# Kernel tuning notes

Measured on AMD Instinct MI355X. Metric: run time of the kernel, lower is better.

The kernel has to match this reference:

```python
import jax, jax.numpy as jnp
import numpy as np

N, E, F_IN, HID, H, NCLS, L = 100000, 1600000, 128, 128, 4, 40, 2
C = HID // H  # per-head channels = 32
LN_EPS = 1e-5
SOFTMAX_EPS = 1e-16  # PyG softmax denominator epsilon


def setup_inputs() -> dict:
    key = jax.random.key(0)
    ks = jax.random.split(key, 8)
    s = 1.0 / np.sqrt(F_IN).astype(np.float32)
    return {
        "x": jax.random.normal(ks[0], (N, F_IN), jnp.float32),
        "edge_index": jax.random.randint(ks[1], (2, E), 0, N, jnp.int32),
        "Wq": jax.random.normal(ks[2], (L, F_IN, HID), jnp.float32) * s,
        "bq": jnp.zeros((L, HID), jnp.float32),
        "Wk": jax.random.normal(ks[3], (L, F_IN, HID), jnp.float32) * s,
        "bk": jnp.zeros((L, HID), jnp.float32),
        "Wv": jax.random.normal(ks[4], (L, F_IN, HID), jnp.float32) * s,
        "bv": jnp.zeros((L, HID), jnp.float32),
        "Ws": jax.random.normal(ks[5], (L, F_IN, HID), jnp.float32) * s,
        "bs": jnp.zeros((L, HID), jnp.float32),
        "gamma": jnp.ones((L, HID), jnp.float32),
        "beta": jnp.zeros((L, HID), jnp.float32),
        "Wout": jax.random.normal(ks[6], (HID, NCLS), jnp.float32) * (1.0 / np.sqrt(HID).astype(np.float32)),
        "bout": jnp.zeros((NCLS,), jnp.float32),
    }


def _transformer_conv(x, src, dst, Wq, bq, Wk, bk, Wv, bv, Ws, bs):
    # PyG TransformerConv, concat=False, root_weight=True, beta=False
    n = x.shape[0]
    q = (x @ Wq + bq).reshape(n, H, C)
    k = (x @ Wk + bk).reshape(n, H, C)
    v = (x @ Wv + bv).reshape(n, H, C)
    # per-edge attention logits: [E, H]
    alpha = jnp.einsum('ehc,ehc->eh', q[dst], k[src]) / np.sqrt(C).astype(np.float32)
    # segment softmax over incoming edges of each destination node
    amax = jax.ops.segment_max(alpha, dst, num_segments=n)        # [N, H]
    ex = jnp.exp(alpha - amax[dst])                               # [E, H]
    denom = jax.ops.segment_sum(ex, dst, num_segments=n)         # [N, H]
    w = ex / (denom[dst] + SOFTMAX_EPS)                           # [E, H]
    msg = v[src] * w[:, :, None]                                  # [E, H, C]
    out = jax.ops.segment_sum(msg, dst, num_segments=n)          # [N, H, C]
    out = out.mean(axis=1)                                        # concat=False -> head average, [N, C*?]. Here C*H==HID only via mean over H of C dims -> [N, C]
    # NOTE: concat=False averages heads -> [N, C]; skip proj maps in->C? In PyG, out_channels=hidden here,
    # so lin_* are Linear(in, heads*hidden)... but TransformerConv(in, hidden) means out_channels=hidden/?
    return out


def _conv(x, src, dst, Wq, bq, Wk, bk, Wv, bv, Ws, bs):
    # Faithful version with out_channels = HID per head? No: TransformerConv(in, hidden, heads, concat=False)
    # in PyG uses out_channels=hidden and lin_* : in -> heads*out_channels. To keep HID total width we model
    # per-head dim C = HID // H (standard multi-head factorization with same total width HID).
    n = x.shape[0]
    q = (x @ Wq + bq).reshape(n, H, C)
    k = (x @ Wk + bk).reshape(n, H, C)
    v = (x @ Wv + bv).reshape(n, H, C)
    alpha = jnp.einsum('ehc,ehc->eh', q[dst], k[src]) / np.sqrt(C).astype(np.float32)
    amax = jax.ops.segment_max(alpha, dst, num_segments=n)
    ex = jnp.exp(alpha - amax[dst])
    denom = jax.ops.segment_sum(ex, dst, num_segments=n)
    w = ex / (denom[dst] + SOFTMAX_EPS)
    msg = (v[src] * w[:, :, None]).reshape(-1, H * C)             # [E, HID]
    agg = jax.ops.segment_sum(msg, dst, num_segments=n)          # [N, HID]
    # concat=False -> mean over heads, then broadcast back is not what PyG does; PyG yields [N, out_channels].
    out = agg.reshape(n, H, C).mean(axis=1)                       # [N, C]
    out = jnp.tile(out, (1, H))                                   # widen back to HID? No — instead use skip of width HID.
    return out


def _conv_layer(x, src, dst, Wq, bq, Wk, bk, Wv, bv, Ws, bs):
    """TransformerConv(in, HID, heads=H, concat=False): lin_{q,k,v}: in -> H*HID is too wide for a
    memory target, so we use the equivalent standard factorization HID = H*C (per-head C), giving
    attention output [N, H, C]; concat=False head-mean is applied per head group and the result is
    projected residually via lin_skip (in -> HID)."""
    n = x.shape[0]
    q = (x @ Wq + bq).reshape(n, H, C)
    k = (x @ Wk + bk).reshape(n, H, C)
    v = (x @ Wv + bv).reshape(n, H, C)
    alpha = jnp.einsum('ehc,ehc->eh', q[dst], k[src]) / np.sqrt(C).astype(np.float32)
    amax = jax.ops.segment_max(alpha, dst, num_segments=n)        # [N, H]
    ex = jnp.exp(alpha - amax[dst])                               # [E, H]
    denom = jax.ops.segment_sum(ex, dst, num_segments=n)
    w = ex / (denom[dst] + SOFTMAX_EPS)
    msg = (v[src] * w[:, :, None]).reshape(-1, HID)               # [E, HID] (head-concat)
    agg = jax.ops.segment_sum(msg, dst, num_segments=n)          # [N, HID]
    return agg + x @ Ws + bs                                      # root/skip connection


def _layernorm(h, g, b):
    mu = h.mean(-1, keepdims=True)
    var = ((h - mu) ** 2).mean(-1, keepdims=True)
    return (h - mu) * jax.lax.rsqrt(var + LN_EPS) * g + b


def reference(x, edge_index, Wq, bq, Wk, bk, Wv, bv, Ws, bs, gamma, beta, Wout, bout):
    src, dst = edge_index[0], edge_index[1]
    h = x
    for l in range(L):  # fixed small layer count
        h = _conv_layer(h, src, dst, Wq[l], bq[l], Wk[l], bk[l], Wv[l], bv[l], Ws[l], bs[l])
        h = jax.nn.relu(_layernorm(h, gamma[l], beta[l]))
        # dropout is identity in eval mode
    return h @ Wout + bout  # [N, NCLS]
```

## Files before the change

### kernel.cpp

```cpp
#include <hip/hip_runtime.h>
#include <math.h>

#define N_NODES 100000
#define N_EDGES 1600000
#define NCLS_ 40
#define NSCAN_BLOCKS ((N_NODES + 1023) / 1024)
#define DRANGE 12500

typedef short bf16x8 __attribute__((ext_vector_type(8)));
typedef float f32x4 __attribute__((ext_vector_type(4)));

__device__ __forceinline__ unsigned short f2b(float f) {
    union { float f; unsigned u; } v; v.f = f;
    unsigned r = v.u + 0x7fffu + ((v.u >> 16) & 1u);
    return (unsigned short)(r >> 16);
}
__device__ __forceinline__ float2 up2(unsigned u) {
    union { unsigned u; float f; } a, b;
    a.u = u << 16; b.u = u & 0xffff0000u;
    return make_float2(a.f, b.f);
}
__device__ __forceinline__ unsigned pk2(float x, float y) {
    return (unsigned)f2b(x) | ((unsigned)f2b(y) << 16);
}
__device__ __forceinline__ float b2f(unsigned short s) {
    union { unsigned u; float f; } v; v.u = ((unsigned)s) << 16;
    return v.f;
}


__global__ void zero_i32_kernel(int* __restrict__ p, int n) {
    int i = blockIdx.x * blockDim.x + threadIdx.x;
    if (i < n) p[i] = 0;
}

__global__ __launch_bounds__(256) void wconv_kernel(
    const float* __restrict__ Wq, const float* __restrict__ Wk,
    const float* __restrict__ Wv, const float* __restrict__ Ws,
    unsigned short* __restrict__ Wbf) {
    int tid = blockIdx.x * 256 + threadIdx.x;
    if (tid >= 131072) return;
    int k   = tid & 127;
    int n   = (tid >> 7) & 63;
    int g   = (tid >> 13) & 1;
    int mat = (tid >> 14) & 3;
    int l   = tid >> 16;
    const float* W = (mat == 0) ? Wq : (mat == 1) ? Wk : (mat == 2) ? Wv : Ws;
    Wbf[tid] = f2b(W[l * 16384 + k * 128 + g * 64 + n]);
}

__global__ __launch_bounds__(256) void hist_kernel(
    const int* __restrict__ dst, int* __restrict__ deg) {
    int group = blockIdx.x & 7;
    int gblk  = blockIdx.x >> 3;
    int nblk  = gridDim.x >> 3;
    int lo = group * DRANGE, hi = lo + DRANGE;
    for (int i = gblk * 256 + threadIdx.x; i < N_EDGES; i += nblk * 256) {
        int d = dst[i];
        if (d >= lo && d < hi) atomicAdd(&deg[d], 1);
    }
}

__global__ __launch_bounds__(1024) void scan_block_kernel(
    const int* __restrict__ deg, int* __restrict__ rowptr, int* __restrict__ sums) {
    __shared__ int tmp[1024];
    int t = threadIdx.x;
    int i = blockIdx.x * 1024 + t;
    int v = (i < N_NODES) ? deg[i] : 0;
    tmp[t] = v;
    __syncthreads();
    for (int d = 1; d < 1024; d <<= 1) {
        int add = (t >= d) ? tmp[t - d] : 0;
        __syncthreads();
        tmp[t] += add;
        __syncthreads();
    }
    if (i < N_NODES) rowptr[i] = tmp[t] - v;
    if (t == 1023) sums[blockIdx.x] = tmp[1023];
}

__global__ __launch_bounds__(128) void scan_sums_kernel(int* __restrict__ sums) {
    __shared__ int tmp[128];
    int t = threadIdx.x;
    int v = (t < NSCAN_BLOCKS) ? sums[t] : 0;
    tmp[t] = v;
    __syncthreads();
    for (int d = 1; d < 128; d <<= 1) {
        int add = (t >= d) ? tmp[t - d] : 0;
        __syncthreads();
        tmp[t] += add;
        __syncthreads();
    }
    if (t < NSCAN_BLOCKS) sums[t] = tmp[t] - v;
}

__global__ void scan_add_kernel(int* __restrict__ rowptr, const int* __restrict__ sums,
                                int* __restrict__ cursor) {
    int i = blockIdx.x * blockDim.x + threadIdx.x;
    if (i < N_NODES) {
        int val = rowptr[i] + sums[i >> 10];
        rowptr[i] = val;
        cursor[i] = val;
    }
    if (i == 0) rowptr[N_NODES] = N_EDGES;
}

__global__ __launch_bounds__(256) void scatter_kernel(
    const int* __restrict__ src, const int* __restrict__ dst,
    int* __restrict__ cursor, int* __restrict__ srcs) {
    int group = blockIdx.x & 7;
    int gblk  = blockIdx.x >> 3;
    int nblk  = gridDim.x >> 3;
    int lo = group * DRANGE, hi = lo + DRANGE;
    for (int i = gblk * 256 + threadIdx.x; i < N_EDGES; i += nblk * 256) {
        int d = dst[i];
        if (d >= lo && d < hi) {
            int pos = atomicAdd(&cursor[d], 1);
            srcs[pos] = src[i];
        }
    }
}

__global__ __launch_bounds__(256) void gemm_qkvs_kernel(
    const void* __restrict__ Ap, int a_is_bf16,
    const unsigned short* __restrict__ Wbf,
    const float* __restrict__ b0, const float* __restrict__ b1,
    const float* __restrict__ b2, const float* __restrict__ b3,
    unsigned short* __restrict__ out) {
    __shared__ unsigned short As[64][138];
    __shared__ unsigned short Bs[2][64][138];
    int t = threadIdx.x;
    int row0 = blockIdx.x * 64;

    if (a_is_bf16) {
        const unsigned short* A = (const unsigned short*)Ap;
        for (int i = 0; i < 8; ++i) {
            int idx = t + i * 256;
            int r = idx >> 5, k4 = (idx & 31) << 2;
            ushort4 v = make_ushort4(0, 0, 0, 0);
            if (row0 + r < N_NODES) v = *(const ushort4*)&A[(size_t)(row0 + r) * 128 + k4];
            *(ushort4*)&As[r][k4] = v;
        }
    } else {
        const float* A = (const float*)Ap;
        for (int i = 0; i < 8; ++i) {
            int idx = t + i * 256;
            int r = idx >> 5, k4 = (idx & 31) << 2;
            float4 v = make_float4(0.f, 0.f, 0.f, 0.f);
            if (row0 + r < N_NODES) v = *(const float4*)&A[(size_t)(row0 + r) * 128 + k4];
            ushort4 o;
            o.x = f2b(v.x); o.y = f2b(v.y); o.z = f2b(v.z); o.w = f2b(v.w);
            *(ushort4*)&As[r][k4] = o;
        }
    }

    int wv = t >> 6, lane = t & 63;
    int ln = lane & 15, quad = lane >> 4;

    ushort4 pf[8];
    {
        const unsigned short* Wg = Wbf;
        for (int i = 0; i < 8; ++i) {
            int idx = t + i * 256;
            pf[i] = *(const ushort4*)&Wg[((idx >> 5) << 7) + ((idx & 31) << 2)];
        }
        for (int i = 0; i < 8; ++i) {
            int idx = t + i * 256;
            *(ushort4*)&Bs[0][idx >> 5][(idx & 31) << 2] = pf[i];
        }
    }
    __syncthreads();

    #pragma unroll
    for (int g = 0; g < 8; ++g) {
        int mat = g >> 1;
        int cur = g & 1;
        const float* bias = (mat == 0) ? b0 : (mat == 1) ? b1 : (mat == 2) ? b2 : b3;
        int cb = (g & 1) * 64;

        if (g < 7) {
            const unsigned short* Wg = Wbf + (size_t)(g + 1) * 8192;
            for (int i = 0; i < 8; ++i) {
                int idx = t + i * 256;
                pf[i] = *(const ushort4*)&Wg[((idx >> 5) << 7) + ((idx & 31) << 2)];
            }
        }

        f32x4 acc[4];
        for (int c = 0; c < 4; ++c) acc[c] = (f32x4){0.f, 0.f, 0.f, 0.f};
        for (int ks = 0; ks < 4; ++ks) {
            int k0 = ks * 32 + quad * 8;
            bf16x8 a = *(bf16x8*)&As[wv * 16 + ln][k0];
            for (int c = 0; c < 4; ++c) {
                bf16x8 b = *(bf16x8*)&Bs[cur][c * 16 + ln][k0];
                acc[c] = __builtin_amdgcn_mfma_f32_16x16x32_bf16(a, b, acc[c], 0, 0, 0);
            }
        }

        for (int c = 0; c < 4; ++c) {
            int colInMat = cb + c * 16 + ln;
            float bb = bias[colInMat];
            int pos;
            if (mat == 0)      pos = colInMat;
            else if (mat == 3) pos = 384 + colInMat;
            else               pos = 128 + ((colInMat >> 2) << 3) + ((mat == 2) ? 4 : 0) + (colInMat & 3);
            for (int r = 0; r < 4; ++r) {
                int row = row0 + wv * 16 + quad * 4 + r;
                if (row < N_NODES)
                    out[(size_t)row * 512 + pos] = f2b(acc[c][r] + bb);
            }
        }

        if (g < 7) {
            int nxt = cur ^ 1;
            for (int i = 0; i < 8; ++i) {
                int idx = t + i * 256;
                *(ushort4*)&Bs[nxt][idx >> 5][(idx & 31) << 2] = pf[i];
            }
        }
        __syncthreads();
    }
}

__global__ __launch_bounds__(256) void edge_fused_kernel(
    const unsigned short* __restrict__ qkvs,
    const int* __restrict__ srcs, const int* __restrict__ rowptr,
    const float* __restrict__ gamma, const float* __restrict__ beta,
    unsigned short* __restrict__ hout) {
    int n = (blockIdx.x * 256 + threadIdx.x) >> 6;
    int lane = threadIdx.x & 63;
    if (n >= N_NODES) return;
    int half = lane >> 5, hl = lane & 31;
    const unsigned short* qrow = qkvs + (size_t)n * 512;
    uint2 qu = *(const uint2*)&qrow[4 * hl];
    float2 q01 = up2(qu.x), q23 = up2(qu.y);
    uint2 su = *(const uint2*)&qrow[384 + 4 * hl];
    float2 sk01 = up2(su.x), sk23 = up2(su.y);
    int e0 = rowptr[n], e1 = rowptr[n + 1];
    float a0 = 0.f, a1 = 0.f, a2 = 0.f, a3 = 0.f, dsum = 0.f;
    const float sc = 0.17677669529663687f;
    int idx = e0;
    for (; idx + 3 < e1; idx += 4) {
        int sA = srcs[idx + half];
        int sB = srcs[idx + 2 + half];
        uint4 kvA = *(const uint4*)&qkvs[(size_t)sA * 512 + 128 + 8 * hl];
        uint4 kvB = *(const uint4*)&qkvs[(size_t)sB * 512 + 128 + 8 * hl];
        float2 kA01 = up2(kvA.x), kA23 = up2(kvA.y);
        float2 kB01 = up2(kvB.x), kB23 = up2(kvB.y);
        float pA = q01.x * kA01.x + q01.y * kA01.y + q23.x * kA23.x + q23.y * kA23.y;
        float pB = q01.x * kB01.x + q01.y * kB01.y + q23.x * kB23.x + q23.y * kB23.y;
        pA += __shfl_xor(pA, 1); pB += __shfl_xor(pB, 1);
        pA += __shfl_xor(pA, 2); pB += __shfl_xor(pB, 2);
        pA += __shfl_xor(pA, 4); pB += __shfl_xor(pB, 4);
        float eA = __expf(pA * sc), eB = __expf(pB * sc);
        float2 vA01 = up2(kvA.z), vA23 = up2(kvA.w);
        float2 vB01 = up2(kvB.z), vB23 = up2(kvB.w);
        a0 += eA * vA01.x + eB * vB01.x;
        a1 += eA * vA01.y + eB * vB01.y;
        a2 += eA * vA23.x + eB * vB23.x;
        a3 += eA * vA23.y + eB * vB23.y;
        dsum += eA + eB;
    }
    for (; idx < e1; idx += 2) {
        int i = idx + half;
        bool valid = i < e1;
        int sA = srcs[valid ? i : e1 - 1];
        uint4 kvA = *(const uint4*)&qkvs[(size_t)sA * 512 + 128 + 8 * hl];
        float2 kA01 = up2(kvA.x), kA23 = up2(kvA.y);
        float pA = q01.x * kA01.x + q01.y * kA01.y + q23.x * kA23.x + q23.y * kA23.y;
        pA += __shfl_xor(pA, 1);
        pA += __shfl_xor(pA, 2);
        pA += __shfl_xor(pA, 4);
        float eA = valid ? __expf(pA * sc) : 0.f;
        float2 vA01 = up2(kvA.z), vA23 = up2(kvA.w);
        a0 += eA * vA01.x; a1 += eA * vA01.y;
        a2 += eA * vA23.x; a3 += eA * vA23.y;
        dsum += eA;
    }
    a0 += __shfl_xor(a0, 32); a1 += __shfl_xor(a1, 32);
    a2 += __shfl_xor(a2, 32); a3 += __shfl_xor(a3, 32);
    dsum += __shfl_xor(dsum, 32);
    float dinv = 1.0f / (dsum + 1e-16f);
    float o0 = a0 * dinv + sk01.x, o1 = a1 * dinv + sk01.y;
    float o2 = a2 * dinv + sk23.x, o3 = a3 * dinv + sk23.y;
    float sum = o0 + o1 + o2 + o3;
    for (int m = 1; m < 64; m <<= 1) sum += __shfl_xor(sum, m);
    float mu = sum * (1.0f / 256.0f);
    float d0 = o0 - mu, d1 = o1 - mu, d2 = o2 - mu, d3 = o3 - mu;
    float sq = d0 * d0 + d1 * d1 + d2 * d2 + d3 * d3;
    for (int m = 1; m < 64; m <<= 1) sq += __shfl_xor(sq, m);
    float rs = rsqrtf(sq * (1.0f / 256.0f) + 1e-5f);
    if (half == 0) {
        float4 g4 = *(const float4*)&gamma[4 * hl];
        float4 b4 = *(const float4*)&beta[4 * hl];
        float r0 = fmaxf(d0 * rs * g4.x + b4.x, 0.f);
        float r1 = fmaxf(d1 * rs * g4.y + b4.y, 0.f);
        float r2 = fmaxf(d2 * rs * g4.z + b4.z, 0.f);
        float r3 = fmaxf(d3 * rs * g4.w + b4.w, 0.f);
        uint2 w;
        w.x = pk2(r0, r1);
        w.y = pk2(r2, r3);
        *(uint2*)&hout[(size_t)n * 128 + 4 * hl] = w;
    }
}

__global__ __launch_bounds__(256) void out_gemm_kernel(
    const unsigned short* __restrict__ h, const float* __restrict__ Wout,
    const float* __restrict__ bout, float* __restrict__ out) {
    __shared__ float hs[32][132];
    __shared__ float ws[128 * NCLS_];
    __shared__ float bsd[NCLS_];
    int t = threadIdx.x;
    int n0 = blockIdx.x * 32;
    for (int i = t; i < 128 * NCLS_; i += 256) ws[i] = Wout[i];
    if (t < NCLS_) bsd[t] = bout[t];
    for (int i = t; i < 1024; i += 256) {
        int r = i >> 5, k4 = (i & 31) << 2;
        float4 a = make_float4(0.f, 0.f, 0.f, 0.f);
        if (n0 + r < N_NODES) {
            ushort4 u = *(const ushort4*)&h[(size_t)(n0 + r) * 128 + k4];
            a = make_float4(b2f(u.x), b2f(u.y), b2f(u.z), b2f(u.w));
        }
        *(float4*)&hs[r][k4] = a;
    }
    __syncthreads();
    int r = t >> 3, j0 = (t & 7) * 5;
    float acc[5];
    for (int j = 0; j < 5; ++j) acc[j] = bsd[j0 + j];
    for (int k = 0; k < 128; ++k) {
        float a = hs[r][k];
        for (int j = 0; j < 5; ++j) acc[j] += a * ws[k * NCLS_ + j0 + j];
    }
    int n = n0 + r;
    if (n < N_NODES) {
        for (int j = 0; j < 5; ++j) out[(size_t)n * NCLS_ + j0 + j] = acc[j];
    }
}

extern "C" void kernel_launch(void* const* d_in, const int* in_sizes, int n_in,
                              void* d_out, int out_size, void* d_ws, size_t ws_size,
                              hipStream_t stream) {
    const float* x    = (const float*)d_in[0];
    const int*   ei   = (const int*)d_in[1];
    const int*   src  = ei;
    const int*   dst  = ei + N_EDGES;
    const float* Wq   = (const float*)d_in[2];
    const float* bq   = (const float*)d_in[3];
    const float* Wk   = (const float*)d_in[4];
    const float* bk   = (const float*)d_in[5];
    const float* Wv   = (const float*)d_in[6];
    const float* bv   = (const float*)d_in[7];
    const float* Wsk  = (const float*)d_in[8];
    const float* bsk  = (const float*)d_in[9];
    const float* gmm  = (const float*)d_in[10];
    const float* bta  = (const float*)d_in[11];
    const float* Wout = (const float*)d_in[12];
    const float* bout = (const float*)d_in[13];
    float* outp = (float*)d_out;

    char* p = (char*)d_ws;
    auto carve = [&](size_t bytes) {
        char* r = p;
        p += (bytes + 255) & ~(size_t)255;
        return r;
    };
    unsigned short* qkvs = (unsigned short*)carve((size_t)N_NODES * 512 * 2);
    unsigned short* h    = (unsigned short*)carve((size_t)N_NODES * 128 * 2);
    unsigned short* Wbf  = (unsigned short*)carve((size_t)131072 * 2);
    int* deg     = (int*)carve((size_t)N_NODES * 4);
    int* rowptr  = (int*)carve((size_t)(N_NODES + 1) * 4);
    int* cursor  = (int*)carve((size_t)N_NODES * 4);
    int* srcs    = (int*)carve((size_t)N_EDGES * 4);
    int* sums    = (int*)carve((size_t)NSCAN_BLOCKS * 4);

    wconv_kernel<<<512, 256, 0, stream>>>(Wq, Wk, Wv, Wsk, Wbf);

    zero_i32_kernel<<<(N_NODES + 255) / 256, 256, 0, stream>>>(deg, N_NODES);
    hist_kernel<<<2048, 256, 0, stream>>>(dst, deg);
    scan_block_kernel<<<NSCAN_BLOCKS, 1024, 0, stream>>>(deg, rowptr, sums);
    scan_sums_kernel<<<1, 128, 0, stream>>>(sums);
    scan_add_kernel<<<(N_NODES + 255) / 256, 256, 0, stream>>>(rowptr, sums, cursor);
    scatter_kernel<<<2048, 256, 0, stream>>>(src, dst, cursor, srcs);

    for (int l = 0; l < 2; ++l) {
        const void* hin = l ? (const void*)h : (const void*)x;
        gemm_qkvs_kernel<<<(N_NODES + 63) / 64, 256, 0, stream>>>(
            hin, l, Wbf + (size_t)l * 65536,
            bq + l * 128, bk + l * 128, bv + l * 128, bsk + l * 128, qkvs);
        edge_fused_kernel<<<(N_NODES + 3) / 4, 256, 0, stream>>>(
            qkvs, srcs, rowptr, gmm + l * 128, bta + l * 128, h);
    }
    out_gemm_kernel<<<(N_NODES + 31) / 32, 256, 0, stream>>>(h, Wout, bout, outp);
}
```

Before: 699.1 us.

## Pad CSR rows to multiples of four, pre-scale offsets, fold softmax scale into Wq

Each node's CSR segment is padded to a multiple of four and the padding is zero-filled. Source indices are stored pre-shifted as byte offsets (src<<10), so the edge loop can issue int4 loads of four neighbours and four K/V gathers per iteration. The 1/sqrt(C)*log2(e) factor is folded into the Wq weights and bias so the kernel uses a hardware exp2 with no per-edge multiply. The output GEMM is rewritten as one node per lane with register-held rows and direct Wout reads. The cost is a larger srcs buffer, an extra zeroing kernel, more padded gather work on low-degree nodes, and reliance on deg and padding for loop bounds.

```diff
diff --git a/kernel.cpp b/kernel.cpp
--- a/kernel.cpp
+++ b/kernel.cpp
@@ -6,6 +6,15 @@
 #define NCLS_ 40
 #define NSCAN_BLOCKS ((N_NODES + 1023) / 1024)
 #define DRANGE 12500
+#define SRCS_PAD (N_EDGES + 3 * N_NODES + 64)
+
+#define QSCALE (0.17677669529663687f * 1.4426950408889634f)
+
+#if __has_builtin(__builtin_amdgcn_exp2f)
+#define EXP2(x) __builtin_amdgcn_exp2f(x)
+#else
+#define EXP2(x) exp2f(x)
+#endif
 
 typedef short bf16x8 __attribute__((ext_vector_type(8)));
 typedef float f32x4 __attribute__((ext_vector_type(4)));
@@ -46,7 +55,9 @@
     int mat = (tid >> 14) & 3;
     int l   = tid >> 16;
     const float* W = (mat == 0) ? Wq : (mat == 1) ? Wk : (mat == 2) ? Wv : Ws;
-    Wbf[tid] = f2b(W[l * 16384 + k * 128 + g * 64 + n]);
+    float w = W[l * 16384 + k * 128 + g * 64 + n];
+    if (mat == 0) w *= QSCALE;
+    Wbf[tid] = f2b(w);
 }
 
 __global__ __launch_bounds__(256) void hist_kernel(
@@ -66,7 +77,7 @@
     __shared__ int tmp[1024];
     int t = threadIdx.x;
     int i = blockIdx.x * 1024 + t;
-    int v = (i < N_NODES) ? deg[i] : 0;
+    int v = (i < N_NODES) ? ((deg[i] + 3) & ~3) : 0;
     tmp[t] = v;
     __syncthreads();
     for (int d = 1; d < 1024; d <<= 1) {
@@ -102,7 +113,6 @@
         rowptr[i] = val;
         cursor[i] = val;
     }
-    if (i == 0) rowptr[N_NODES] = N_EDGES;
 }
 
 __global__ __launch_bounds__(256) void scatter_kernel(
@@ -116,7 +126,7 @@
         int d = dst[i];
         if (d >= lo && d < hi) {
             int pos = atomicAdd(&cursor[d], 1);
-            srcs[pos] = src[i];
+            srcs[pos] = src[i] << 10;
         }
     }
 }
@@ -200,6 +210,7 @@
         for (int c = 0; c < 4; ++c) {
             int colInMat = cb + c * 16 + ln;
             float bb = bias[colInMat];
+            if (mat == 0) bb *= QSCALE;
             int pos;
             if (mat == 0)      pos = colInMat;
             else if (mat == 3) pos = 384 + colInMat;
@@ -222,9 +233,22 @@
     }
 }
 
+#define EDGE(KV, ECOND) {                                            \
+        float2 k01 = up2(KV.x), k23 = up2(KV.y);                     \
+        float p = q01.x*k01.x + q01.y*k01.y + q23.x*k23.x + q23.y*k23.y; \
+        p += __shfl_xor(p, 1);                                       \
+        p += __shfl_xor(p, 2);                                       \
+        p += __shfl_xor(p, 4);                                       \
+        float e = (ECOND);                                           \
+        float2 v01 = up2(KV.z), v23 = up2(KV.w);                     \
+        a0 = fmaf(e, v01.x, a0); a1 = fmaf(e, v01.y, a1);            \
+        a2 = fmaf(e, v23.x, a2); a3 = fmaf(e, v23.y, a3);            \
+        dsum += e; }
+
 __global__ __launch_bounds__(256) void edge_fused_kernel(
     const unsigned short* __restrict__ qkvs,
     const int* __restrict__ srcs, const int* __restrict__ rowptr,
+    const int* __restrict__ deg,
     const float* __restrict__ gamma, const float* __restrict__ beta,
     unsigned short* __restrict__ hout) {
     int n = (blockIdx.x * 256 + threadIdx.x) >> 6;
@@ -236,47 +260,39 @@
     float2 q01 = up2(qu.x), q23 = up2(qu.y);
     uint2 su = *(const uint2*)&qrow[384 + 4 * hl];
     float2 sk01 = up2(su.x), sk23 = up2(su.y);
-    int e0 = rowptr[n], e1 = rowptr[n + 1];
+    int e0 = rowptr[n];
+    int rem = deg[n];
+    const char* kbase = (const char*)qkvs + 256 + 16 * hl;
+    const int* sb = srcs + e0 + 4 * half;
     float a0 = 0.f, a1 = 0.f, a2 = 0.f, a3 = 0.f, dsum = 0.f;
-    const float sc = 0.17677669529663687f;
-    int idx = e0;
-    for (; idx + 3 < e1; idx += 4) {
-        int sA = srcs[idx + half];
-        int sB = srcs[idx + 2 + half];
-        uint4 kvA = *(const uint4*)&qkvs[(size_t)sA * 512 + 128 + 8 * hl];
-        uint4 kvB = *(const uint4*)&qkvs[(size_t)sB * 512 + 128 + 8 * hl];
-        float2 kA01 = up2(kvA.x), kA23 = up2(kvA.y);
-        float2 kB01 = up2(kvB.x), kB23 = up2(kvB.y);
-        float pA = q01.x * kA01.x + q01.y * kA01.y + q23.x * kA23.x + q23.y * kA23.y;
-        float pB = q01.x * kB01.x + q01.y * kB01.y + q23.x * kB23.x + q23.y * kB23.y;
-        pA += __shfl_xor(pA, 1); pB += __shfl_xor(pB, 1);
-        pA += __shfl_xor(pA, 2); pB += __shfl_xor(pB, 2);
-        pA += __shfl_xor(pA, 4); pB += __shfl_xor(pB, 4);
-        float eA = __expf(pA * sc), eB = __expf(pB * sc);
-        float2 vA01 = up2(kvA.z), vA23 = up2(kvA.w);
-        float2 vB01 = up2(kvB.z), vB23 = up2(kvB.w);
-        a0 += eA * vA01.x + eB * vB01.x;
-        a1 += eA * vA01.y + eB * vB01.y;
-        a2 += eA * vA23.x + eB * vB23.x;
-        a3 += eA * vA23.y + eB * vB23.y;
-        dsum += eA + eB;
-    }
-    for (; idx < e1; idx += 2) {
-        int i = idx + half;
-        bool valid = i < e1;
-        int sA = srcs[valid ? i : e1 - 1];
-        uint4 kvA = *(const uint4*)&qkvs[(size_t)sA * 512 + 128 + 8 * hl];
-        float2 kA01 = up2(kvA.x), kA23 = up2(kvA.y);
-        float pA = q01.x * kA01.x + q01.y * kA01.y + q23.x * kA23.x + q23.y * kA23.y;
-        pA += __shfl_xor(pA, 1);
-        pA += __shfl_xor(pA, 2);
-        pA += __shfl_xor(pA, 4);
-        float eA = valid ? __expf(pA * sc) : 0.f;
-        float2 vA01 = up2(kvA.z), vA23 = up2(kvA.w);
-        a0 += eA * vA01.x; a1 += eA * vA01.y;
-        a2 += eA * vA23.x; a3 += eA * vA23.y;
-        dsum += eA;
-    }
+
+    int4 oc;
+    if (rem >= 8) oc = *(const int4*)sb;
+    while (rem >= 8) {
+        int4 on = *(const int4*)(sb + 8);
+        uint4 kv0 = *(const uint4*)(kbase + (unsigned)oc.x);
+        uint4 kv1 = *(const uint4*)(kbase + (unsigned)oc.y);
+        uint4 kv2 = *(const uint4*)(kbase + (unsigned)oc.z);
+        uint4 kv3 = *(const uint4*)(kbase + (unsigned)oc.w);
+        EDGE(kv0, EXP2(p));
+        EDGE(kv1, EXP2(p));
+        EDGE(kv2, EXP2(p));
+        EDGE(kv3, EXP2(p));
+        oc = on; sb += 8; rem -= 8;
+    }
+    if (rem > 0) {
+        int4 ot = *(const int4*)sb;
+        int tb = 4 * half;
+        uint4 kv0 = *(const uint4*)(kbase + (unsigned)ot.x);
+        uint4 kv1 = *(const uint4*)(kbase + (unsigned)ot.y);
+        uint4 kv2 = *(const uint4*)(kbase + (unsigned)ot.z);
+        uint4 kv3 = *(const uint4*)(kbase + (unsigned)ot.w);
+        EDGE(kv0, (tb + 0 < rem) ? EXP2(p) : 0.f);
+        EDGE(kv1, (tb + 1 < rem) ? EXP2(p) : 0.f);
+        EDGE(kv2, (tb + 2 < rem) ? EXP2(p) : 0.f);
+        EDGE(kv3, (tb + 3 < rem) ? EXP2(p) : 0.f);
+    }
+
     a0 += __shfl_xor(a0, 32); a1 += __shfl_xor(a1, 32);
     a2 += __shfl_xor(a2, 32); a3 += __shfl_xor(a3, 32);
     dsum += __shfl_xor(dsum, 32);
@@ -307,33 +323,40 @@
 __global__ __launch_bounds__(256) void out_gemm_kernel(
     const unsigned short* __restrict__ h, const float* __restrict__ Wout,
     const float* __restrict__ bout, float* __restrict__ out) {
-    __shared__ float hs[32][132];
-    __shared__ float ws[128 * NCLS_];
-    __shared__ float bsd[NCLS_];
-    int t = threadIdx.x;
-    int n0 = blockIdx.x * 32;
-    for (int i = t; i < 128 * NCLS_; i += 256) ws[i] = Wout[i];
-    if (t < NCLS_) bsd[t] = bout[t];
-    for (int i = t; i < 1024; i += 256) {
-        int r = i >> 5, k4 = (i & 31) << 2;
-        float4 a = make_float4(0.f, 0.f, 0.f, 0.f);
-        if (n0 + r < N_NODES) {
-            ushort4 u = *(const ushort4*)&h[(size_t)(n0 + r) * 128 + k4];
-            a = make_float4(b2f(u.x), b2f(u.y), b2f(u.z), b2f(u.w));
-        }
-        *(float4*)&hs[r][k4] = a;
-    }
-    __syncthreads();
-    int r = t >> 3, j0 = (t & 7) * 5;
-    float acc[5];
-    for (int j = 0; j < 5; ++j) acc[j] = bsd[j0 + j];
-    for (int k = 0; k < 128; ++k) {
-        float a = hs[r][k];
-        for (int j = 0; j < 5; ++j) acc[j] += a * ws[k * NCLS_ + j0 + j];
-    }
-    int n = n0 + r;
+    int wv = __builtin_amdgcn_readfirstlane((int)(threadIdx.x >> 6));
+    int l = threadIdx.x & 63;
+    int n = blockIdx.x * 64 + l;
+    int jb = wv * 10;
+    int nc = (n < N_NODES) ? n : (N_NODES - 1);
+    const unsigned short* hrow = h + (size_t)nc * 128;
+    uint4 hp[16];
+    #pragma unroll
+    for (int i = 0; i < 16; ++i) hp[i] = *(const uint4*)&hrow[i * 8];
+    float acc[10];
+    #pragma unroll
+    for (int j = 0; j < 10; ++j) acc[j] = bout[jb + j];
+    #pragma unroll
+    for (int i = 0; i < 16; ++i) {
+        float2 c01 = up2(hp[i].x), c23 = up2(hp[i].y);
+        float2 c45 = up2(hp[i].z), c67 = up2(hp[i].w);
+        float hc0 = c01.x, hc1 = c01.y, hc2 = c23.x, hc3 = c23.y;
+        float hc4 = c45.x, hc5 = c45.y, hc6 = c67.x, hc7 = c67.y;
+        #pragma unroll
+        for (int j = 0; j < 10; ++j) {
+            const float* wk = Wout + (i * 8) * NCLS_ + jb + j;
+            acc[j] = fmaf(hc0, wk[0 * NCLS_], acc[j]);
+            acc[j] = fmaf(hc1, wk[1 * NCLS_], acc[j]);
+            acc[j] = fmaf(hc2, wk[2 * NCLS_], acc[j]);
+            acc[j] = fmaf(hc3, wk[3 * NCLS_], acc[j]);
+            acc[j] = fmaf(hc4, wk[4 * NCLS_], acc[j]);
+            acc[j] = fmaf(hc5, wk[5 * NCLS_], acc[j]);
+            acc[j] = fmaf(hc6, wk[6 * NCLS_], acc[j]);
+            acc[j] = fmaf(hc7, wk[7 * NCLS_], acc[j]);
+        }
+    }
     if (n < N_NODES) {
-        for (int j = 0; j < 5; ++j) out[(size_t)n * NCLS_ + j0 + j] = acc[j];
+        #pragma unroll
+        for (int j = 0; j < 10; ++j) out[(size_t)n * NCLS_ + jb + j] = acc[j];
     }
 }
 
@@ -370,12 +393,13 @@
     int* deg     = (int*)carve((size_t)N_NODES * 4);
     int* rowptr  = (int*)carve((size_t)(N_NODES + 1) * 4);
     int* cursor  = (int*)carve((size_t)N_NODES * 4);
-    int* srcs    = (int*)carve((size_t)N_EDGES * 4);
+    int* srcs    = (int*)carve((size_t)SRCS_PAD * 4);
     int* sums    = (int*)carve((size_t)NSCAN_BLOCKS * 4);
 
     wconv_kernel<<<512, 256, 0, stream>>>(Wq, Wk, Wv, Wsk, Wbf);
 
     zero_i32_kernel<<<(N_NODES + 255) / 256, 256, 0, stream>>>(deg, N_NODES);
+    zero_i32_kernel<<<(SRCS_PAD + 255) / 256, 256, 0, stream>>>(srcs, SRCS_PAD);
     hist_kernel<<<2048, 256, 0, stream>>>(dst, deg);
     scan_block_kernel<<<NSCAN_BLOCKS, 1024, 0, stream>>>(deg, rowptr, sums);
     scan_sums_kernel<<<1, 128, 0, stream>>>(sums);
@@ -388,7 +412,7 @@
             hin, l, Wbf + (size_t)l * 65536,
             bq + l * 128, bk + l * 128, bv + l * 128, bsk + l * 128, qkvs);
         edge_fused_kernel<<<(N_NODES + 3) / 4, 256, 0, stream>>>(
-            qkvs, srcs, rowptr, gmm + l * 128, bta + l * 128, h);
-    }
-    out_gemm_kernel<<<(N_NODES + 31) / 32, 256, 0, stream>>>(h, Wout, bout, outp);
-}
+            qkvs, srcs, rowptr, deg, gmm + l * 128, bta + l * 128, h);
+    }
+    out_gemm_kernel<<<(N_NODES + 63) / 64, 256, 0, stream>>>(h, Wout, bout, outp);
+}
```

Measured after the change: 711.2 us. No clear change (+1.7%).
